# Optimization experiments

Hardware: AMD Instinct MI355X
Metric: run time of the kernel (lower is better)

The kernel has to match this reference:

```python
import jax, jax.numpy as jnp
import numpy as np

# Problem constants (would come from parameter_group in the original module)
N_POS = 512      # number of scan positions
BATCH = 32       # diffraction patterns per batch
N_OPR = 4        # OPR (orthogonal probe relaxation) modes
N_MODES = 8      # incoherent probe modes
H_OBJ = W_OBJ = 1024
HP = WP = 256    # probe / patch size
N_SLICES = 4     # multislice object
WAVELENGTH = 1.24e-10   # m (10 keV X-rays)
PIXEL = 1.0e-8          # m object pixel size
DZ = 2.0e-6             # m slice spacing


def _as_complex(x):
    return jax.lax.complex(x[..., 0], x[..., 1])


def _angular_spectrum_tf():
    # Transfer function H(fx,fy) = exp(i*dz*kz), kz = 2*pi/lambda * sqrt(1-(l*fx)^2-(l*fy)^2)
    fy = np.fft.fftfreq(HP, d=PIXEL)
    fx = np.fft.fftfreq(WP, d=PIXEL)
    FY, FX = np.meshgrid(fy, fx, indexing='ij')
    arg = 1.0 - (WAVELENGTH * FX) ** 2 - (WAVELENGTH * FY) ** 2
    kz = 2.0 * np.pi / WAVELENGTH * np.sqrt(np.maximum(arg, 0.0))
    tf = np.exp(1j * DZ * kz) * (arg > 0)  # evanescent cutoff
    return jnp.asarray(tf, jnp.complex64)

_TF = _angular_spectrum_tf()


def setup_inputs() -> dict:
    key = jax.random.key(0)
    k1, k2, k3, k4, k5 = jax.random.split(key, 5)
    object_ri = jax.random.normal(k1, (N_SLICES, H_OBJ, W_OBJ, 2), jnp.float32) * 0.1
    # make object roughly a weak phase/amplitude modulator around 1
    object_ri = object_ri.at[..., 0].add(1.0)
    probe_ri = jax.random.normal(k2, (N_OPR, N_MODES, HP, WP, 2), jnp.float32)
    opr_weights = jax.random.normal(k3, (N_POS, N_OPR), jnp.float32) * 0.1
    opr_weights = opr_weights.at[:, 0].add(1.0)
    # positions (row, col) such that the 256x256 patch fits inside the object
    positions = jax.random.uniform(k4, (N_POS, 2), jnp.float32,
                                   minval=16.0, maxval=float(H_OBJ - HP - 16))
    indices = jax.random.randint(k5, (BATCH,), 0, N_POS, jnp.int32)
    return {"object_ri": object_ri, "probe_ri": probe_ri,
            "opr_weights": opr_weights, "positions": positions, "indices": indices}


def reference(object_ri, probe_ri, opr_weights, positions, indices):
    obj = _as_complex(object_ri)      # (S, H, W)
    probe = _as_complex(probe_ri)     # (K, M, h, w)
    pos = positions[indices]          # (B, 2)
    rpos = jnp.round(pos)
    frac = pos - rpos                 # fractional shifts compensated on probe
    ipos = rpos.astype(jnp.int32)

    # --- gather object patches at rounded positions: (B, S, h, w) ---
    def get_patch(rc):
        return jax.lax.dynamic_slice(obj, (0, rc[0], rc[1]), (N_SLICES, HP, WP))
    patches = jax.vmap(get_patch)(ipos)

    # --- unique probes via OPR weighting of mode 0 ---
    w = opr_weights[indices].astype(probe.dtype)           # (B, K)
    p0 = jnp.einsum('bk,khw->bhw', w, probe[:, 0])         # (B, h, w)
    pk = jnp.broadcast_to(probe[0, 1:], (pos.shape[0], N_MODES - 1, HP, WP))
    uprobe = jnp.concatenate([p0[:, None], pk], axis=1)    # (B, M, h, w)

    # --- subpixel Fourier shift of probes by fractional positions ---
    fy = jnp.fft.fftfreq(HP).astype(jnp.float32)
    fx = jnp.fft.fftfreq(WP).astype(jnp.float32)
    ramp = frac[:, 0, None, None] * fy[:, None] + frac[:, 1, None, None] * fx[None, :]
    phase = jnp.exp(jax.lax.complex(jnp.zeros_like(ramp), -2.0 * jnp.pi * ramp))  # (B, h, w)
    uprobe = jnp.fft.ifft2(jnp.fft.fft2(uprobe) * phase[:, None])

    # --- multislice propagation through the object ---
    psi = uprobe
    for s in range(N_SLICES):
        psi = patches[:, s, None] * psi                    # modulate
        if s < N_SLICES - 1:
            psi = jnp.fft.ifft2(jnp.fft.fft2(psi) * _TF)   # angular spectrum

    # --- far-field (Fourier) propagation to detector ---
    psi_far = jnp.fft.fftshift(
        jnp.fft.fft2(jnp.fft.ifftshift(psi, axes=(-2, -1)), norm='ortho'),
        axes=(-2, -1))
    # incoherent sum over probe modes -> detector intensities (B, h, w)
    return jnp.sum(jnp.abs(psi_far) ** 2, axis=1)
```

## Files before the change

kernel.cpp:

```cpp
#include <hip/hip_runtime.h>
#include <hip/hip_fp16.h>
#include <math.h>

#define HP 256
#define NB 32
#define NM 8
#define NK 4
#define NS 4
#define HOBJ 1024

__device__ __forceinline__ float2 cmul(float2 a, float2 b) {
    return make_float2(fmaf(a.x, b.x, -a.y * b.y), fmaf(a.x, b.y, a.y * b.x));
}

__device__ __forceinline__ float2 h2f(__half2 h) {
    return make_float2(__low2float(h), __high2float(h));
}
__device__ __forceinline__ __half2 f2h(float2 v) {
    return __floats2half2_rn(v.x, v.y);
}

__constant__ float COS16[10] = {1.f, 0.9238795325f, 0.7071067812f, 0.3826834324f, 0.f,
                                -0.3826834324f, -0.7071067812f, -0.9238795325f, -1.f, -0.9238795325f};
__constant__ float SIN16[10] = {0.f, 0.3826834324f, 0.7071067812f, 0.9238795325f, 1.f,
                                0.9238795325f, 0.7071067812f, 0.3826834324f, 0.f, -0.3826834324f};

template <int S>
__device__ __forceinline__ void dft4(float2 a, float2 b, float2 c, float2 d,
                                     float2* o0, float2* o1, float2* o2, float2* o3) {
    float2 apc = make_float2(a.x + c.x, a.y + c.y);
    float2 amc = make_float2(a.x - c.x, a.y - c.y);
    float2 bpd = make_float2(b.x + d.x, b.y + d.y);
    float2 bmd = make_float2(b.x - d.x, b.y - d.y);
    float2 ib = (S < 0) ? make_float2(bmd.y, -bmd.x) : make_float2(-bmd.y, bmd.x);
    *o0 = make_float2(apc.x + bpd.x, apc.y + bpd.y);
    *o1 = make_float2(amc.x + ib.x, amc.y + ib.y);
    *o2 = make_float2(apc.x - bpd.x, apc.y - bpd.y);
    *o3 = make_float2(amc.x - ib.x, amc.y - ib.y);
}

template <int S>
__device__ __forceinline__ void fft16(float2 v[16]) {
    float2 t[16];
#pragma unroll
    for (int b = 0; b < 4; ++b)
        dft4<S>(v[b], v[4 + b], v[8 + b], v[12 + b],
                &t[4 * b + 0], &t[4 * b + 1], &t[4 * b + 2], &t[4 * b + 3]);
#pragma unroll
    for (int b = 1; b < 4; ++b)
#pragma unroll
        for (int c = 1; c < 4; ++c) {
            int j = b * c;
            float2 w = make_float2(COS16[j], (S < 0) ? -SIN16[j] : SIN16[j]);
            t[4 * b + c] = cmul(t[4 * b + c], w);
        }
#pragma unroll
    for (int c = 0; c < 4; ++c)
        dft4<S>(t[c], t[4 + c], t[8 + c], t[12 + c],
                &v[c + 0], &v[c + 4], &v[c + 8], &v[c + 12]);
}

__device__ __forceinline__ float2 twiddle_base(int S, int t) {
    float sn, cs;
    __sincosf((float)S * 0.0245436926f  * (float)t, &sn, &cs);
    return make_float2(cs, sn);
}

template <int S>
__device__ __forceinline__ void fft256_w(float2 v[16], int t, float* lds) {
    fft16<S>(v);
    float2 base = twiddle_base(S, t);
    float2 cur = base;
#pragma unroll
    for (int k = 1; k < 16; ++k) {
        v[k] = cmul(v[k], cur);
        cur = cmul(cur, base);
    }
    asm volatile("" ::: "memory");
#pragma unroll
    for (int k = 0; k < 16; ++k) lds[k * 17 + t] = v[k].x;
    asm volatile("" ::: "memory");
#pragma unroll
    for (int j = 0; j < 16; ++j) v[j].x = lds[t * 17 + j];
    asm volatile("" ::: "memory");
#pragma unroll
    for (int k = 0; k < 16; ++k) lds[k * 17 + t] = v[k].y;
    asm volatile("" ::: "memory");
#pragma unroll
    for (int j = 0; j < 16; ++j) v[j].y = lds[t * 17 + j];
    fft16<S>(v);
}

template <int S>
__device__ __forceinline__ void fft256_b(float2 v[16], int t, float* ldsRe, float* ldsIm) {
    fft16<S>(v);
    float2 base = twiddle_base(S, t);
    float2 cur = base;
#pragma unroll
    for (int k = 1; k < 16; ++k) {
        v[k] = cmul(v[k], cur);
        cur = cmul(cur, base);
    }
    __syncthreads();
#pragma unroll
    for (int k = 0; k < 16; ++k) {
        ldsRe[k * 17 + t] = v[k].x;
        ldsIm[k * 17 + t] = v[k].y;
    }
    __syncthreads();
#pragma unroll
    for (int j = 0; j < 16; ++j) {
        v[j].x = ldsRe[t * 17 + j];
        v[j].y = ldsIm[t * 17 + j];
    }
    fft16<S>(v);
}

#define ROWSTRIDE 272
#define COLSTRIDE 290

__global__ void k_init_shared(const float* __restrict__ probe, float2* __restrict__ sharedK) {
    __shared__ float sc[16 * ROWSTRIDE];
    int tt = threadIdx.x;
    int t = tt & 15, g = tt >> 4;
    int rowg = blockIdx.x, m = blockIdx.y + 1;
    int y = rowg * 16 + g;
    const float2* p = (const float2*)probe + (size_t)m * 65536 + (size_t)y * 256;
    float2 v[16];
#pragma unroll
    for (int n1 = 0; n1 < 16; ++n1) v[n1] = p[n1 * 16 + t];
    fft256_w<-1>(v, t, &sc[g * ROWSTRIDE]);
    float2* ob = sharedK + (size_t)(m - 1) * 65536 + (size_t)y * 256;
#pragma unroll
    for (int k2 = 0; k2 < 16; ++k2) ob[k2 * 16 + t] = v[k2];
}

__global__ void k_init_m0(const float* __restrict__ probe, const float* __restrict__ opr_w,
                          const int* __restrict__ indices, __half2* __restrict__ buf, int b0) {
    __shared__ float sc[16 * ROWSTRIDE];
    int tt = threadIdx.x;
    int t = tt & 15, g = tt >> 4;
    int rowg = blockIdx.x, bl = blockIdx.z;
    int b = b0 + bl;
    int y = rowg * 16 + g;
    int idx = indices[b];
    float w0 = opr_w[idx * 4 + 0], w1 = opr_w[idx * 4 + 1];
    float w2 = opr_w[idx * 4 + 2], w3 = opr_w[idx * 4 + 3];
    const float2* p = (const float2*)probe;
    size_t rb = (size_t)y * 256;
    float2 v[16];
#pragma unroll
    for (int n1 = 0; n1 < 16; ++n1) {
        size_t o = rb + n1 * 16 + t;
        float2 p0 = p[o];
        float2 p1 = p[(size_t)(1 * NM) * 65536 + o];
        float2 p2 = p[(size_t)(2 * NM) * 65536 + o];
        float2 p3 = p[(size_t)(3 * NM) * 65536 + o];
        v[n1] = make_float2(w0 * p0.x + w1 * p1.x + w2 * p2.x + w3 * p3.x,
                            w0 * p0.y + w1 * p1.y + w2 * p2.y + w3 * p3.y);
    }
    fft256_w<-1>(v, t, &sc[g * ROWSTRIDE]);
    __half2* ob = buf + (size_t)(bl * NM) * 65536 + (size_t)y * 256;
#pragma unroll
    for (int k2 = 0; k2 < 16; ++k2) ob[k2 * 16 + t] = f2h(v[k2]);
}

__global__ void k_col_shift(const float* __restrict__ positions, const int* __restrict__ indices,
                            const float2* __restrict__ sharedK, __half2* __restrict__ buf, int b0) {
    __shared__ float sRe[16 * COLSTRIDE], sIm[16 * COLSTRIDE];
    int tt = threadIdx.x;
    int c = tt & 15, t = tt >> 4;
    int colg = blockIdx.x, m = blockIdx.y, bl = blockIdx.z;
    int b = b0 + bl;
    int x = colg * 16 + c;
    int idx = indices[b];
    float py = positions[idx * 2 + 0], px = positions[idx * 2 + 1];
    float fr0 = py - rintf(py), fr1 = px - rintf(px);
    float2 v[16];
    if (m) {
        const float2* src = sharedK + (size_t)(m - 1) * 65536;
#pragma unroll
        for (int n1 = 0; n1 < 16; ++n1) v[n1] = src[(size_t)(n1 * 16 + t) * 256 + x];
    } else {
        const __half2* src = buf + (size_t)(bl * NM) * 65536;
#pragma unroll
        for (int n1 = 0; n1 < 16; ++n1) v[n1] = h2f(src[(size_t)(n1 * 16 + t) * 256 + x]);
    }
    __half2* dst = buf + (size_t)(bl * NM + m) * 65536;
    fft256_b<-1>(v, t, &sRe[c * COLSTRIDE], &sIm[c * COLSTRIDE]);
    float fxv = (float)((x < 128) ? x : x - 256) * (1.0f / 256.0f);
    float fy0 = (float)t * (1.0f / 256.0f);
    float sn, cs;
    __sincosf(-6.2831853071795864769f * (fr0 * fy0 + fr1 * fxv), &sn, &cs);
    float2 cur = make_float2(cs, sn);
    __sincosf(-6.2831853071795864769f * fr0 * (1.0f / 16.0f), &sn, &cs);
    float2 step = make_float2(cs, sn);
    __sincosf(6.2831853071795864769f * fr0, &sn, &cs);
    float2 wrap = make_float2(cs, sn);
#pragma unroll
    for (int k2 = 0; k2 < 16; ++k2) {
        if (k2 == 8) cur = cmul(cur, wrap);
        v[k2] = cmul(v[k2], cur);
        cur = cmul(cur, step);
    }
    fft256_b<1>(v, t, &sRe[c * COLSTRIDE], &sIm[c * COLSTRIDE]);
#pragma unroll
    for (int j = 0; j < 16; ++j) {
        float2 r = make_float2(v[j].x * (1.0f / 256.0f), v[j].y * (1.0f / 256.0f));
        dst[(size_t)(j * 16 + t) * 256 + x] = f2h(r);
    }
}

__global__ void k_row_prop(const float* __restrict__ object, const float* __restrict__ positions,
                           const int* __restrict__ indices, __half2* __restrict__ buf, int b0, int s) {
    __shared__ float sc[16 * ROWSTRIDE];
    int tt = threadIdx.x;
    int t = tt & 15, g = tt >> 4;
    int rowg = blockIdx.x, m = blockIdx.y, bl = blockIdx.z;
    int b = b0 + bl;
    int y = rowg * 16 + g;
    int idx = indices[b];
    int r0 = (int)rintf(positions[idx * 2 + 0]);
    int r1 = (int)rintf(positions[idx * 2 + 1]);
    __half2* img = buf + (size_t)(bl * NM + m) * 65536 + (size_t)y * 256;
    float2 v[16];
#pragma unroll
    for (int n1 = 0; n1 < 16; ++n1) v[n1] = h2f(img[n1 * 16 + t]);
    fft256_w<1>(v, t, &sc[g * ROWSTRIDE]);
    const float2* obj = (const float2*)object + (size_t)s * HOBJ * HOBJ + (size_t)(r0 + y) * HOBJ + r1;
#pragma unroll
    for (int j = 0; j < 16; ++j) {
        int xx = t + 16 * j;
        float2 pz = obj[xx];
        float2 ps = make_float2(v[j].x * (1.0f / 256.0f), v[j].y * (1.0f / 256.0f));
        v[j] = cmul(ps, pz);
    }
    fft256_w<-1>(v, t, &sc[g * ROWSTRIDE]);
#pragma unroll
    for (int k2 = 0; k2 < 16; ++k2) img[k2 * 16 + t] = f2h(v[k2]);
}

__global__ void k_col_tf(const float2* __restrict__ tf, __half2* __restrict__ buf) {
    __shared__ float sRe[16 * COLSTRIDE], sIm[16 * COLSTRIDE];
    int tt = threadIdx.x;
    int c = tt & 15, t = tt >> 4;
    int colg = blockIdx.x, m = blockIdx.y, bl = blockIdx.z;
    int x = colg * 16 + c;
    __half2* img = buf + (size_t)(bl * NM + m) * 65536;
    float2 v[16];
#pragma unroll
    for (int n1 = 0; n1 < 16; ++n1) v[n1] = h2f(img[(size_t)(n1 * 16 + t) * 256 + x]);
    fft256_b<-1>(v, t, &sRe[c * COLSTRIDE], &sIm[c * COLSTRIDE]);
#pragma unroll
    for (int k2 = 0; k2 < 16; ++k2) {
        int ky = t + 16 * k2;
        v[k2] = cmul(v[k2], tf[ky * 256 + x]);
    }
    fft256_b<1>(v, t, &sRe[c * COLSTRIDE], &sIm[c * COLSTRIDE]);
#pragma unroll
    for (int j = 0; j < 16; ++j) {
        float2 r = make_float2(v[j].x * (1.0f / 256.0f), v[j].y * (1.0f / 256.0f));
        img[(size_t)(j * 16 + t) * 256 + x] = f2h(r);
    }
}

__global__ void k_col_final(const __half2* __restrict__ buf, float* __restrict__ out,
                            float* __restrict__ part, int b0) {
    __shared__ float sRe[16 * COLSTRIDE], sIm[16 * COLSTRIDE];
    int tt = threadIdx.x;
    int c = tt & 15, t = tt >> 4;
    int colg = blockIdx.x, mp = blockIdx.y, bl = blockIdx.z;
    int x = colg * 16 + c;
    float acc[16];
#pragma unroll
    for (int j = 0; j < 16; ++j) acc[j] = 0.f;
#pragma unroll
    for (int mi = 0; mi < 4; ++mi) {
        int m = mp * 4 + mi;
        const __half2* img = buf + (size_t)(bl * NM + m) * 65536;
        float2 v[16];
#pragma unroll
        for (int n1 = 0; n1 < 16; ++n1) v[n1] = h2f(img[(size_t)(n1 * 16 + t) * 256 + x]);
        fft256_b<-1>(v, t, &sRe[c * COLSTRIDE], &sIm[c * COLSTRIDE]);
#pragma unroll
        for (int k2 = 0; k2 < 16; ++k2)
            acc[k2] = fmaf(v[k2].x, v[k2].x, fmaf(v[k2].y, v[k2].y, acc[k2]));
    }
    int b = b0 + bl;
    float* ob = (mp ? part : out) + (size_t)b * 65536;
    int xs = (x + 128) & 255;
#pragma unroll
    for (int k2 = 0; k2 < 16; ++k2) {
        int ky = t + 16 * k2;
        int ys = (ky + 128) & 255;
        ob[ys * 256 + xs] = acc[k2] * (1.0f / 65536.0f);
    }
}

__global__ void k_addout(float* __restrict__ out, const float* __restrict__ part) {
    int i = blockIdx.x * 256 + threadIdx.x;
    float4 a = ((const float4*)out)[i];
    float4 p = ((const float4*)part)[i];
    ((float4*)out)[i] = make_float4(a.x + p.x, a.y + p.y, a.z + p.z, a.w + p.w);
}

__global__ void k_tf(float2* __restrict__ tf) {
    int i = blockIdx.x * 256 + threadIdx.x;
    int ky = i >> 8, kx = i & 255;
    double fy = (double)((ky < 128) ? ky : ky - 256) / (256.0 * 1.0e-8);
    double fx = (double)((kx < 128) ? kx : kx - 256) / (256.0 * 1.0e-8);
    double ly = 1.24e-10 * fy, lx = 1.24e-10 * fx;
    double arg = 1.0 - lx * lx - ly * ly;
    float2 r = make_float2(0.f, 0.f);
    if (arg > 0.0) {
        double kz = (2.0 * M_PI / 1.24e-10) * sqrt(arg);
        double ph = 2.0e-6 * kz;
        r = make_float2((float)cos(ph), (float)sin(ph));
    }
    tf[i] = r;
}

extern "C" void kernel_launch(void* const* d_in, const int* in_sizes, int n_in,
                              void* d_out, int out_size, void* d_ws, size_t ws_size,
                              hipStream_t stream) {
    const float* object = (const float*)d_in[0];
    const float* probe = (const float*)d_in[1];
    const float* opr_w = (const float*)d_in[2];
    const float* positions = (const float*)d_in[3];
    const int* indices = (const int*)d_in[4];
    float* out = (float*)d_out;

    float2* tf = (float2*)d_ws;
    float2* sharedK = (float2*)((char*)d_ws + ((size_t)1 << 20));
    float* part = (float*)((char*)d_ws + ((size_t)8 << 20));
    __half2* buf = (__half2*)((char*)d_ws + ((size_t)16 << 20));
    size_t head = (size_t)16 << 20;
    size_t avail = (ws_size > head) ? ws_size - head : 0;
    long long perb = (long long)NM * 65536 * sizeof(__half2);
    int Bc = (int)(avail / perb);
    if (Bc > NB) Bc = NB;
    if (Bc < 1) Bc = 1;

    k_tf<<<256, 256, 0, stream>>>(tf);
    k_init_shared<<<dim3(16, NM - 1, 1), 256, 0, stream>>>(probe, sharedK);

    for (int b0 = 0; b0 < NB; b0 += Bc) {
        int bc = (NB - b0 < Bc) ? (NB - b0) : Bc;
        dim3 grid(16, NM, bc);
        k_init_m0<<<dim3(16, 1, bc), 256, 0, stream>>>(probe, opr_w, indices, buf, b0);
        k_col_shift<<<grid, 256, 0, stream>>>(positions, indices, sharedK, buf, b0);
        for (int s = 0; s < NS; ++s) {
            k_row_prop<<<grid, 256, 0, stream>>>(object, positions, indices, buf, b0, s);
            if (s < NS - 1) k_col_tf<<<grid, 256, 0, stream>>>(tf, buf);
        }
        dim3 gridE(16, 2, bc);
        k_col_final<<<gridE, 256, 0, stream>>>(buf, out, part, b0);
    }
    k_addout<<<(NB * 65536) / (256 * 4), 256, 0, stream>>>(out, part);
}
```

Before: 401.0 us.

## Fuse probe init, shift and multislice passes into one per-image megakernel

Replaces the chain of separate init, column-shift, row-propagation and column-TF kernels with one kernel in which a 512-thread block holds an entire 256x256 image in registers as half2. Column FFTs are done by transposing through shared memory, and the transfer function is stored transposed so each column reads it contiguously. This removes repeated global-memory round trips of the intermediate wavefield and many kernel launches. The cost is only NM*bc blocks (256 for the full batch), heavy register pressure from the 128-entry half2 array, and many block-wide syncs per transpose, which may hurt occupancy.

```diff
diff --git a/kernel.cpp b/kernel.cpp
--- a/kernel.cpp
+++ b/kernel.cpp
@@ -12,7 +12,6 @@
 __device__ __forceinline__ float2 cmul(float2 a, float2 b) {
     return make_float2(fmaf(a.x, b.x, -a.y * b.y), fmaf(a.x, b.y, a.y * b.x));
 }
-
 __device__ __forceinline__ float2 h2f(__half2 h) {
     return make_float2(__low2float(h), __high2float(h));
 }
@@ -119,8 +118,183 @@
 #define ROWSTRIDE 272
 #define COLSTRIDE 290
 
+
+__device__ __forceinline__ void transposeA(__half2 (&D)[8][16], int g, int t,
+                                           __half2 (*T)[257]) {
+#pragma unroll
+    for (int c = 0; c < 8; ++c) {
+        __syncthreads();
+#pragma unroll
+        for (int k = 0; k < 16; ++k) T[g][16 * k + t] = D[c][k];
+        __syncthreads();
+#pragma unroll
+        for (int j = 0; j < 2; ++j)
+#pragma unroll
+            for (int cc = 0; cc < 8; ++cc)
+                D[c][2 * cc + j] = T[16 * j + t][g + 32 * cc];
+    }
+    __syncthreads();
+}
+
+__device__ __forceinline__ void transposeB(__half2 (&D)[8][16], int g, int t,
+                                           __half2 (*T)[257]) {
+#pragma unroll
+    for (int c = 0; c < 8; ++c) {
+        __syncthreads();
+#pragma unroll
+        for (int k = 0; k < 16; ++k) T[g][16 * k + t] = D[k >> 1][2 * c + (k & 1)];
+        __syncthreads();
+#pragma unroll
+        for (int j = 0; j < 2; ++j)
+#pragma unroll
+            for (int cc = 0; cc < 8; ++cc)
+                D[cc][2 * c + j] = T[16 * j + t][g + 32 * cc];
+    }
+    __syncthreads();
+}
+
+__global__ __launch_bounds__(512) void k_mega(
+        const float* __restrict__ probe, const float* __restrict__ opr_w,
+        const float2* __restrict__ sharedK, const float* __restrict__ object,
+        const float* __restrict__ positions, const int* __restrict__ indices,
+        const float2* __restrict__ tfT, __half2* __restrict__ buf, int b0) {
+    __shared__ __align__(16) char UB[34816];
+    float* sc = (float*)UB;
+    __half2 (*T)[257] = (__half2(*)[257])UB;
+
+    int tt = threadIdx.x;
+    int t = tt & 15, g = tt >> 4;
+    int m = blockIdx.x, bl = blockIdx.y;
+    int b = b0 + bl;
+    float* scg = sc + g * 272;
+
+    int idx = indices[b];
+    float py = positions[idx * 2 + 0], px = positions[idx * 2 + 1];
+    float fr0 = py - rintf(py), fr1 = px - rintf(px);
+    int r0 = (int)rintf(py), r1 = (int)rintf(px);
+
+    __half2 D[8][16];
+    float2 v[16];
+
+    if (m == 0) {
+        float w0 = opr_w[idx * 4 + 0], w1 = opr_w[idx * 4 + 1];
+        float w2 = opr_w[idx * 4 + 2], w3 = opr_w[idx * 4 + 3];
+        const float2* p = (const float2*)probe;
+#pragma unroll
+        for (int r = 0; r < 8; ++r) {
+            int y = g + 32 * r;
+            size_t rb = (size_t)y * 256;
+#pragma unroll
+            for (int n = 0; n < 16; ++n) {
+                size_t o = rb + n * 16 + t;
+                float2 p0 = p[o];
+                float2 p1 = p[(size_t)(1 * NM) * 65536 + o];
+                float2 p2 = p[(size_t)(2 * NM) * 65536 + o];
+                float2 p3 = p[(size_t)(3 * NM) * 65536 + o];
+                v[n] = make_float2(w0 * p0.x + w1 * p1.x + w2 * p2.x + w3 * p3.x,
+                                   w0 * p0.y + w1 * p1.y + w2 * p2.y + w3 * p3.y);
+            }
+            fft256_w<-1>(v, t, scg);
+#pragma unroll
+            for (int k = 0; k < 16; ++k) D[r][k] = f2h(v[k]);
+        }
+    } else {
+        const float2* sk = sharedK + (size_t)(m - 1) * 65536;
+#pragma unroll
+        for (int r = 0; r < 8; ++r) {
+            int y = g + 32 * r;
+#pragma unroll
+            for (int k = 0; k < 16; ++k)
+                D[r][k] = f2h(sk[(size_t)y * 256 + 16 * k + t]);
+        }
+    }
+
+    transposeA(D, g, t, T);
+
+    {
+        float fy0 = (float)t * (1.0f / 256.0f);
+        float sn, cs;
+        __sincosf(-6.2831853071795864769f * fr0 * (1.0f / 16.0f), &sn, &cs);
+        float2 step = make_float2(cs, sn);
+        __sincosf(6.2831853071795864769f * fr0, &sn, &cs);
+        float2 wrap = make_float2(cs, sn);
+#pragma unroll
+        for (int a = 0; a < 8; ++a) {
+            int x = g + 32 * a;
+#pragma unroll
+            for (int n = 0; n < 16; ++n) v[n] = h2f(D[n >> 1][2 * a + (n & 1)]);
+            fft256_w<-1>(v, t, scg);
+            float fxv = (float)((x < 128) ? x : x - 256) * (1.0f / 256.0f);
+            __sincosf(-6.2831853071795864769f * (fr0 * fy0 + fr1 * fxv), &sn, &cs);
+            float2 cur = make_float2(cs, sn);
+#pragma unroll
+            for (int k2 = 0; k2 < 16; ++k2) {
+                if (k2 == 8) cur = cmul(cur, wrap);
+                v[k2] = cmul(v[k2], cur);
+                cur = cmul(cur, step);
+            }
+            fft256_w<1>(v, t, scg);
+#pragma unroll
+            for (int k = 0; k < 16; ++k)
+                D[k >> 1][2 * a + (k & 1)] =
+                    f2h(make_float2(v[k].x * (1.0f / 256.0f), v[k].y * (1.0f / 256.0f)));
+        }
+    }
+
+    transposeB(D, g, t, T);
+
+    __half2* ob = buf + (size_t)(bl * NM + m) * 65536;
+
+    for (int s = 0; s < NS; ++s) {
+        const float2* obase = (const float2*)object + (size_t)s * HOBJ * HOBJ;
+#pragma unroll
+        for (int r = 0; r < 8; ++r) {
+            int y = g + 32 * r;
+#pragma unroll
+            for (int n = 0; n < 16; ++n) v[n] = h2f(D[r][n]);
+            fft256_w<1>(v, t, scg);
+            const float2* orow = obase + (size_t)(r0 + y) * HOBJ + r1;
+#pragma unroll
+            for (int j = 0; j < 16; ++j) {
+                float2 pz = orow[t + 16 * j];
+                float2 ps = make_float2(v[j].x * (1.0f / 256.0f), v[j].y * (1.0f / 256.0f));
+                v[j] = cmul(ps, pz);
+            }
+            fft256_w<-1>(v, t, scg);
+            if (s == NS - 1) {
+#pragma unroll
+                for (int k = 0; k < 16; ++k)
+                    ob[(size_t)y * 256 + 16 * k + t] = f2h(v[k]);
+            } else {
+#pragma unroll
+                for (int k = 0; k < 16; ++k) D[r][k] = f2h(v[k]);
+            }
+        }
+        if (s < NS - 1) {
+            transposeA(D, g, t, T);
+#pragma unroll
+            for (int a = 0; a < 8; ++a) {
+                int x = g + 32 * a;
+#pragma unroll
+                for (int n = 0; n < 16; ++n) v[n] = h2f(D[n >> 1][2 * a + (n & 1)]);
+                fft256_w<-1>(v, t, scg);
+                const float2* tcol = tfT + (size_t)x * 256;
+#pragma unroll
+                for (int k2 = 0; k2 < 16; ++k2)
+                    v[k2] = cmul(v[k2], tcol[t + 16 * k2]);
+                fft256_w<1>(v, t, scg);
+#pragma unroll
+                for (int k = 0; k < 16; ++k)
+                    D[k >> 1][2 * a + (k & 1)] =
+                        f2h(make_float2(v[k].x * (1.0f / 256.0f), v[k].y * (1.0f / 256.0f)));
+            }
+            transposeB(D, g, t, T);
+        }
+    }
+}
+
 __global__ void k_init_shared(const float* __restrict__ probe, float2* __restrict__ sharedK) {
-    __shared__ float sc[16 * ROWSTRIDE];
+    __shared__ float scm[16 * ROWSTRIDE];
     int tt = threadIdx.x;
     int t = tt & 15, g = tt >> 4;
     int rowg = blockIdx.x, m = blockIdx.y + 1;
@@ -129,139 +303,10 @@
     float2 v[16];
 #pragma unroll
     for (int n1 = 0; n1 < 16; ++n1) v[n1] = p[n1 * 16 + t];
-    fft256_w<-1>(v, t, &sc[g * ROWSTRIDE]);
+    fft256_w<-1>(v, t, &scm[g * ROWSTRIDE]);
     float2* ob = sharedK + (size_t)(m - 1) * 65536 + (size_t)y * 256;
 #pragma unroll
     for (int k2 = 0; k2 < 16; ++k2) ob[k2 * 16 + t] = v[k2];
-}
-
-__global__ void k_init_m0(const float* __restrict__ probe, const float* __restrict__ opr_w,
-                          const int* __restrict__ indices, __half2* __restrict__ buf, int b0) {
-    __shared__ float sc[16 * ROWSTRIDE];
-    int tt = threadIdx.x;
-    int t = tt & 15, g = tt >> 4;
-    int rowg = blockIdx.x, bl = blockIdx.z;
-    int b = b0 + bl;
-    int y = rowg * 16 + g;
-    int idx = indices[b];
-    float w0 = opr_w[idx * 4 + 0], w1 = opr_w[idx * 4 + 1];
-    float w2 = opr_w[idx * 4 + 2], w3 = opr_w[idx * 4 + 3];
-    const float2* p = (const float2*)probe;
-    size_t rb = (size_t)y * 256;
-    float2 v[16];
-#pragma unroll
-    for (int n1 = 0; n1 < 16; ++n1) {
-        size_t o = rb + n1 * 16 + t;
-        float2 p0 = p[o];
-        float2 p1 = p[(size_t)(1 * NM) * 65536 + o];
-        float2 p2 = p[(size_t)(2 * NM) * 65536 + o];
-        float2 p3 = p[(size_t)(3 * NM) * 65536 + o];
-        v[n1] = make_float2(w0 * p0.x + w1 * p1.x + w2 * p2.x + w3 * p3.x,
-                            w0 * p0.y + w1 * p1.y + w2 * p2.y + w3 * p3.y);
-    }
-    fft256_w<-1>(v, t, &sc[g * ROWSTRIDE]);
-    __half2* ob = buf + (size_t)(bl * NM) * 65536 + (size_t)y * 256;
-#pragma unroll
-    for (int k2 = 0; k2 < 16; ++k2) ob[k2 * 16 + t] = f2h(v[k2]);
-}
-
-__global__ void k_col_shift(const float* __restrict__ positions, const int* __restrict__ indices,
-                            const float2* __restrict__ sharedK, __half2* __restrict__ buf, int b0) {
-    __shared__ float sRe[16 * COLSTRIDE], sIm[16 * COLSTRIDE];
-    int tt = threadIdx.x;
-    int c = tt & 15, t = tt >> 4;
-    int colg = blockIdx.x, m = blockIdx.y, bl = blockIdx.z;
-    int b = b0 + bl;
-    int x = colg * 16 + c;
-    int idx = indices[b];
-    float py = positions[idx * 2 + 0], px = positions[idx * 2 + 1];
-    float fr0 = py - rintf(py), fr1 = px - rintf(px);
-    float2 v[16];
-    if (m) {
-        const float2* src = sharedK + (size_t)(m - 1) * 65536;
-#pragma unroll
-        for (int n1 = 0; n1 < 16; ++n1) v[n1] = src[(size_t)(n1 * 16 + t) * 256 + x];
-    } else {
-        const __half2* src = buf + (size_t)(bl * NM) * 65536;
-#pragma unroll
-        for (int n1 = 0; n1 < 16; ++n1) v[n1] = h2f(src[(size_t)(n1 * 16 + t) * 256 + x]);
-    }
-    __half2* dst = buf + (size_t)(bl * NM + m) * 65536;
-    fft256_b<-1>(v, t, &sRe[c * COLSTRIDE], &sIm[c * COLSTRIDE]);
-    float fxv = (float)((x < 128) ? x : x - 256) * (1.0f / 256.0f);
-    float fy0 = (float)t * (1.0f / 256.0f);
-    float sn, cs;
-    __sincosf(-6.2831853071795864769f * (fr0 * fy0 + fr1 * fxv), &sn, &cs);
-    float2 cur = make_float2(cs, sn);
-    __sincosf(-6.2831853071795864769f * fr0 * (1.0f / 16.0f), &sn, &cs);
-    float2 step = make_float2(cs, sn);
-    __sincosf(6.2831853071795864769f * fr0, &sn, &cs);
-    float2 wrap = make_float2(cs, sn);
-#pragma unroll
-    for (int k2 = 0; k2 < 16; ++k2) {
-        if (k2 == 8) cur = cmul(cur, wrap);
-        v[k2] = cmul(v[k2], cur);
-        cur = cmul(cur, step);
-    }
-    fft256_b<1>(v, t, &sRe[c * COLSTRIDE], &sIm[c * COLSTRIDE]);
-#pragma unroll
-    for (int j = 0; j < 16; ++j) {
-        float2 r = make_float2(v[j].x * (1.0f / 256.0f), v[j].y * (1.0f / 256.0f));
-        dst[(size_t)(j * 16 + t) * 256 + x] = f2h(r);
-    }
-}
-
-__global__ void k_row_prop(const float* __restrict__ object, const float* __restrict__ positions,
-                           const int* __restrict__ indices, __half2* __restrict__ buf, int b0, int s) {
-    __shared__ float sc[16 * ROWSTRIDE];
-    int tt = threadIdx.x;
-    int t = tt & 15, g = tt >> 4;
-    int rowg = blockIdx.x, m = blockIdx.y, bl = blockIdx.z;
-    int b = b0 + bl;
-    int y = rowg * 16 + g;
-    int idx = indices[b];
-    int r0 = (int)rintf(positions[idx * 2 + 0]);
-    int r1 = (int)rintf(positions[idx * 2 + 1]);
-    __half2* img = buf + (size_t)(bl * NM + m) * 65536 + (size_t)y * 256;
-    float2 v[16];
-#pragma unroll
-    for (int n1 = 0; n1 < 16; ++n1) v[n1] = h2f(img[n1 * 16 + t]);
-    fft256_w<1>(v, t, &sc[g * ROWSTRIDE]);
-    const float2* obj = (const float2*)object + (size_t)s * HOBJ * HOBJ + (size_t)(r0 + y) * HOBJ + r1;
-#pragma unroll
-    for (int j = 0; j < 16; ++j) {
-        int xx = t + 16 * j;
-        float2 pz = obj[xx];
-        float2 ps = make_float2(v[j].x * (1.0f / 256.0f), v[j].y * (1.0f / 256.0f));
-        v[j] = cmul(ps, pz);
-    }
-    fft256_w<-1>(v, t, &sc[g * ROWSTRIDE]);
-#pragma unroll
-    for (int k2 = 0; k2 < 16; ++k2) img[k2 * 16 + t] = f2h(v[k2]);
-}
-
-__global__ void k_col_tf(const float2* __restrict__ tf, __half2* __restrict__ buf) {
-    __shared__ float sRe[16 * COLSTRIDE], sIm[16 * COLSTRIDE];
-    int tt = threadIdx.x;
-    int c = tt & 15, t = tt >> 4;
-    int colg = blockIdx.x, m = blockIdx.y, bl = blockIdx.z;
-    int x = colg * 16 + c;
-    __half2* img = buf + (size_t)(bl * NM + m) * 65536;
-    float2 v[16];
-#pragma unroll
-    for (int n1 = 0; n1 < 16; ++n1) v[n1] = h2f(img[(size_t)(n1 * 16 + t) * 256 + x]);
-    fft256_b<-1>(v, t, &sRe[c * COLSTRIDE], &sIm[c * COLSTRIDE]);
-#pragma unroll
-    for (int k2 = 0; k2 < 16; ++k2) {
-        int ky = t + 16 * k2;
-        v[k2] = cmul(v[k2], tf[ky * 256 + x]);
-    }
-    fft256_b<1>(v, t, &sRe[c * COLSTRIDE], &sIm[c * COLSTRIDE]);
-#pragma unroll
-    for (int j = 0; j < 16; ++j) {
-        float2 r = make_float2(v[j].x * (1.0f / 256.0f), v[j].y * (1.0f / 256.0f));
-        img[(size_t)(j * 16 + t) * 256 + x] = f2h(r);
-    }
 }
 
 __global__ void k_col_final(const __half2* __restrict__ buf, float* __restrict__ out,
@@ -304,11 +349,11 @@
     ((float4*)out)[i] = make_float4(a.x + p.x, a.y + p.y, a.z + p.z, a.w + p.w);
 }
 
-__global__ void k_tf(float2* __restrict__ tf) {
+__global__ void k_tf(float2* __restrict__ tfT) {
     int i = blockIdx.x * 256 + threadIdx.x;
-    int ky = i >> 8, kx = i & 255;
+    int x = i >> 8, ky = i & 255;
     double fy = (double)((ky < 128) ? ky : ky - 256) / (256.0 * 1.0e-8);
-    double fx = (double)((kx < 128) ? kx : kx - 256) / (256.0 * 1.0e-8);
+    double fx = (double)((x < 128) ? x : x - 256) / (256.0 * 1.0e-8);
     double ly = 1.24e-10 * fy, lx = 1.24e-10 * fx;
     double arg = 1.0 - lx * lx - ly * ly;
     float2 r = make_float2(0.f, 0.f);
@@ -317,7 +362,7 @@
         double ph = 2.0e-6 * kz;
         r = make_float2((float)cos(ph), (float)sin(ph));
     }
-    tf[i] = r;
+    tfT[i] = r;
 }
 
 extern "C" void kernel_launch(void* const* d_in, const int* in_sizes, int n_in,
@@ -330,7 +375,7 @@
     const int* indices = (const int*)d_in[4];
     float* out = (float*)d_out;
 
-    float2* tf = (float2*)d_ws;
+    float2* tfT = (float2*)d_ws;
     float2* sharedK = (float2*)((char*)d_ws + ((size_t)1 << 20));
     float* part = (float*)((char*)d_ws + ((size_t)8 << 20));
     __half2* buf = (__half2*)((char*)d_ws + ((size_t)16 << 20));
@@ -341,18 +386,13 @@
     if (Bc > NB) Bc = NB;
     if (Bc < 1) Bc = 1;
 
-    k_tf<<<256, 256, 0, stream>>>(tf);
+    k_tf<<<256, 256, 0, stream>>>(tfT);
     k_init_shared<<<dim3(16, NM - 1, 1), 256, 0, stream>>>(probe, sharedK);
 
     for (int b0 = 0; b0 < NB; b0 += Bc) {
         int bc = (NB - b0 < Bc) ? (NB - b0) : Bc;
-        dim3 grid(16, NM, bc);
-        k_init_m0<<<dim3(16, 1, bc), 256, 0, stream>>>(probe, opr_w, indices, buf, b0);
-        k_col_shift<<<grid, 256, 0, stream>>>(positions, indices, sharedK, buf, b0);
-        for (int s = 0; s < NS; ++s) {
-            k_row_prop<<<grid, 256, 0, stream>>>(object, positions, indices, buf, b0, s);
-            if (s < NS - 1) k_col_tf<<<grid, 256, 0, stream>>>(tf, buf);
-        }
+        k_mega<<<dim3(NM, bc), 512, 0, stream>>>(probe, opr_w, sharedK, object,
+                                                 positions, indices, tfT, buf, b0);
         dim3 gridE(16, 2, bc);
         k_col_final<<<gridE, 256, 0, stream>>>(buf, out, part, b0);
     }
```

Measured after the change: 771.6 us. 92.4% more time.
